# Kernel tuning notes

Hardware: AMD Instinct MI355X
Metric: run time of the kernel (lower is better)

Reference implementation:

```python
import jax, jax.numpy as jnp
import numpy as np

D_MODEL, D_STATE, D_CONV, EXPAND = 1024, 16, 4, 2
D_INNER = D_MODEL * EXPAND
B, T = 1, 2048
EPS = 1e-5


def setup_inputs() -> dict:
    key = jax.random.key(0)
    ks = jax.random.split(key, 8)
    x = jax.random.normal(ks[0], (B, T, D_MODEL), dtype=jnp.float32)
    W_in = jax.random.normal(ks[1], (D_MODEL, 2 * D_INNER), dtype=jnp.float32) * 0.02
    conv_w = jax.random.normal(ks[2], (D_INNER, D_CONV), dtype=jnp.float32) * 0.2
    conv_b = jax.random.normal(ks[3], (D_INNER,), dtype=jnp.float32) * 0.02
    W_x = jax.random.normal(ks[4], (D_INNER, 2 * D_STATE + 1), dtype=jnp.float32) * 0.02
    W_dt = jax.random.normal(ks[5], (1, D_INNER), dtype=jnp.float32) * 0.5
    b_dt = jax.random.uniform(ks[6], (D_INNER,), dtype=jnp.float32, minval=-0.001, maxval=0.001)
    A_log = jnp.broadcast_to(jnp.log(jnp.arange(1, D_STATE + 1, dtype=jnp.float32))[None, :], (D_INNER, D_STATE))
    Dparam = jnp.ones((D_INNER,), dtype=jnp.float32)
    W_out = jax.random.normal(ks[7], (D_INNER, D_MODEL), dtype=jnp.float32) * 0.02
    ln_g = jnp.ones((D_MODEL,), dtype=jnp.float32)
    ln_b = jnp.zeros((D_MODEL,), dtype=jnp.float32)
    return {"x": x, "W_in": W_in, "conv_w": conv_w, "conv_b": conv_b, "W_x": W_x,
            "W_dt": W_dt, "b_dt": b_dt, "A_log": A_log, "D": Dparam,
            "W_out": W_out, "ln_g": ln_g, "ln_b": ln_b}


def _silu(v):
    return v * jax.nn.sigmoid(v)


def _layernorm(v, g, b):
    mu = jnp.mean(v, axis=-1, keepdims=True)
    var = jnp.mean((v - mu) ** 2, axis=-1, keepdims=True)
    return (v - mu) * jax.lax.rsqrt(var + EPS) * g + b


def _causal_depthwise_conv(xp, conv_w, conv_b):
    # xp: (B, T, D_INNER) -> (B, D_INNER, T) with left pad of D_CONV-1
    xc = jnp.swapaxes(xp, 1, 2)
    xc = jnp.pad(xc, ((0, 0), (0, 0), (D_CONV - 1, 0)))
    w = conv_w[:, None, :]  # (O=D_INNER, I/groups=1, K)
    out = jax.lax.conv_general_dilated(
        xc, w, window_strides=(1,), padding='VALID',
        dimension_numbers=('NCH', 'OIH', 'NCH'), feature_group_count=D_INNER)
    return jnp.swapaxes(out + conv_b[None, :, None], 1, 2)  # (B, T, D_INNER)


def reference(x, W_in, conv_w, conv_b, W_x, W_dt, b_dt, A_log, D, W_out, ln_g, ln_b):
    residual = x
    xn = _layernorm(x, ln_g, ln_b)
    xz = xn @ W_in                      # (B, T, 2*D_INNER)
    x_proj, z = jnp.split(xz, 2, axis=-1)
    x_conv = _silu(_causal_depthwise_conv(x_proj, conv_w, conv_b))  # (B, T, D_INNER)

    ssm = x_conv @ W_x                  # (B, T, 1 + 2*D_STATE)
    dt_raw = ssm[..., :1]
    Bp = ssm[..., 1:1 + D_STATE]        # (B, T, D_STATE)
    Cp = ssm[..., 1 + D_STATE:]         # (B, T, D_STATE)
    dt = jax.nn.softplus(dt_raw @ W_dt + b_dt)  # (B, T, D_INNER)

    A = -jnp.exp(A_log)                 # (D_INNER, D_STATE)
    A_bar = jnp.exp(dt[..., None] * A)                              # (B,T,d,n)
    Bx = dt[..., None] * Bp[:, :, None, :] * x_conv[..., None]      # (B,T,d,n)

    def step(h, inp):
        Ab_t, Bx_t, C_t = inp           # (B,d,n),(B,d,n),(B,n)
        h = Ab_t * h + Bx_t
        y_t = jnp.einsum('bdn,bn->bd', h, C_t)
        return h, y_t

    h0 = jnp.zeros((x.shape[0], D_INNER, D_STATE), dtype=x.dtype)
    _, ys = jax.lax.scan(step, h0, (jnp.swapaxes(A_bar, 0, 1),
                                    jnp.swapaxes(Bx, 0, 1),
                                    jnp.swapaxes(Cp, 0, 1)))
    y = jnp.swapaxes(ys, 0, 1)          # (B, T, D_INNER)

    y = y + x_conv * D
    y = y * _silu(z)
    return y @ W_out + residual
```

## Files before the change

kernel.cpp:

```cpp
#include <hip/hip_runtime.h>
#include <hip/hip_bf16.h>

typedef __hip_bfloat16 bf16;
typedef __attribute__((ext_vector_type(8))) short bf16x8;
typedef __attribute__((ext_vector_type(4))) float f32x4;

#define T_LEN 2048
#define DMODEL 1024
#define DINNER 2048
#define DSTATE 16
#define LN_EPS 1e-5f
#define NCHUNK 128
#define CLEN 16
#define SSTR 64
#define PSEG 131072

#define GLOBAL_AS __attribute__((address_space(1)))
#define LDS_AS __attribute__((address_space(3)))

__device__ __forceinline__ void g2l16(void* lds, const void* g) {
    __builtin_amdgcn_global_load_lds((const GLOBAL_AS void*)g, (LDS_AS void*)lds, 16, 0, 0);
}

__device__ __forceinline__ float b2f(short s) {
    return __uint_as_float(((unsigned)(unsigned short)s) << 16);
}

__device__ __forceinline__ unsigned short f2bu(float f) {
    bf16 b = __float2bfloat16(f);
    return *reinterpret_cast<unsigned short*>(&b);
}

__global__ void prep_all(const float* __restrict__ Win, const float* __restrict__ Wout,
                         const float* __restrict__ Wx, const float* __restrict__ x,
                         const float* __restrict__ lng, const float* __restrict__ lnb,
                         bf16* __restrict__ WinT, bf16* __restrict__ WoutT,
                         bf16* __restrict__ WxT, bf16* __restrict__ xn) {
    __shared__ float t[32][33];
    int bid = blockIdx.x, tid = threadIdx.x;
    int tx = tid & 31, ty4 = (tid >> 5) * 4;
    if (bid < 4096) {
        int n0 = (bid & 127) * 32, k0 = (bid >> 7) * 32;
#pragma unroll
        for (int r = 0; r < 4; r++)
            t[ty4 + r][tx] = Win[(size_t)(k0 + ty4 + r) * 4096 + n0 + tx];
        __syncthreads();
#pragma unroll
        for (int r = 0; r < 4; r++)
            WinT[(size_t)(n0 + ty4 + r) * 1024 + k0 + tx] = __float2bfloat16(t[tx][ty4 + r]);
    } else if (bid < 6144) {
        int b = bid - 4096;
        int n0 = (b & 31) * 32, k0 = (b >> 5) * 32;
#pragma unroll
        for (int r = 0; r < 4; r++)
            t[ty4 + r][tx] = Wout[(size_t)(k0 + ty4 + r) * 1024 + n0 + tx];
        __syncthreads();
#pragma unroll
        for (int r = 0; r < 4; r++)
            WoutT[(size_t)(n0 + ty4 + r) * 2048 + k0 + tx] = __float2bfloat16(t[tx][ty4 + r]);
    } else if (bid < 6656) {
        int idx = (bid - 6144) * 256 + tid;
        int n = idx >> 11, k = idx & 2047;
        int j = (n == 0) ? 0 : (n >= 4 && n <= 35) ? n - 3 : -1;
        WxT[idx] = __float2bfloat16(j >= 0 ? Wx[k * 33 + j] : 0.f);
    } else {
        int row = bid - 6656;
        const float* xr = x + (size_t)row * DMODEL;
        float v[4];
        float s = 0.f, q = 0.f;
#pragma unroll
        for (int i = 0; i < 4; i++) {
            v[i] = xr[tid + i * 256];
            s += v[i];
            q += v[i] * v[i];
        }
        __shared__ float sh_s[256], sh_q[256];
        sh_s[tid] = s; sh_q[tid] = q;
        __syncthreads();
        for (int st = 128; st > 0; st >>= 1) {
            if (tid < st) { sh_s[tid] += sh_s[tid + st]; sh_q[tid] += sh_q[tid + st]; }
            __syncthreads();
        }
        float mean = sh_s[0] * (1.f / DMODEL);
        float var  = sh_q[0] * (1.f / DMODEL) - mean * mean;
        float rstd = rsqrtf(var + LN_EPS);
#pragma unroll
        for (int i = 0; i < 4; i++) {
            int c = tid + i * 256;
            xn[(size_t)row * DMODEL + c] =
                __float2bfloat16((v[i] - mean) * rstd * lng[c] + lnb[c]);
        }
    }
}

template <int BM, int BN, int WAVE_M, int WAVE_N, int WRITE_RESID, int OUT_BF16>
__global__ void gemm_mfma(const bf16* __restrict__ A, const bf16* __restrict__ Bt,
                          void* __restrict__ Cv, const float* __restrict__ resid,
                          int M, int N, int Kslice, int lda) {
    constexpr int WMsz = BM / WAVE_M;
    constexpr int WNsz = BN / WAVE_N;
    constexpr int TM = WMsz / 16;
    constexpr int TN = WNsz / 16;
    __shared__ short As[BM * 64];
    __shared__ short Bs[BN * 64];
    int tid = threadIdx.x;
    int lane = tid & 63, wave = tid >> 6;
    int wm = (wave / WAVE_N) * WMsz, wn = (wave % WAVE_N) * WNsz;
    int rowBase = blockIdx.y * BM, colBase = blockIdx.x * BN;
    int kbase = blockIdx.z * Kslice;

    f32x4 acc[TM][TN];
#pragma unroll
    for (int i = 0; i < TM; i++)
#pragma unroll
        for (int j = 0; j < TN; j++) acc[i][j] = f32x4{0.f, 0.f, 0.f, 0.f};

    int srow = tid >> 3;
    int cc = (tid & 7) ^ (srow & 7);
    const int ldsoff = tid * 16;

    for (int k0 = kbase; k0 < kbase + Kslice; k0 += 64) {
#pragma unroll
        for (int j = 0; j < BM / 32; j++)
            g2l16((char*)As + j * 4096 + ldsoff,
                  A + (size_t)(rowBase + j * 32 + srow) * lda + k0 + cc * 8);
#pragma unroll
        for (int j = 0; j < BN / 32; j++)
            g2l16((char*)Bs + j * 4096 + ldsoff,
                  Bt + (size_t)(colBase + j * 32 + srow) * lda + k0 + cc * 8);
        __syncthreads();
#pragma unroll
        for (int ks = 0; ks < 2; ks++) {
            bf16x8 af[TM], bfr[TN];
#pragma unroll
            for (int i = 0; i < TM; i++) {
                int row = wm + i * 16 + (lane & 15);
                int slot = (ks * 4 + (lane >> 4)) ^ (row & 7);
                af[i] = *(const bf16x8*)((const char*)As + row * 128 + slot * 16);
            }
#pragma unroll
            for (int j = 0; j < TN; j++) {
                int row = wn + j * 16 + (lane & 15);
                int slot = (ks * 4 + (lane >> 4)) ^ (row & 7);
                bfr[j] = *(const bf16x8*)((const char*)Bs + row * 128 + slot * 16);
            }
#pragma unroll
            for (int i = 0; i < TM; i++)
#pragma unroll
                for (int j = 0; j < TN; j++)
                    acc[i][j] = __builtin_amdgcn_mfma_f32_16x16x32_bf16(
                        af[i], bfr[j], acc[i][j], 0, 0, 0);
        }
        __syncthreads();
    }
    int rq = lane >> 4, cn = lane & 15;
    float* Cf = (float*)Cv + (size_t)blockIdx.z * M * N;
#pragma unroll
    for (int i = 0; i < TM; i++) {
#pragma unroll
        for (int j = 0; j < TN; j++) {
#pragma unroll
            for (int r = 0; r < 4; r++) {
                size_t row = rowBase + wm + i * 16 + rq * 4 + r;
                int col = colBase + wn + j * 16 + cn;
                float v = acc[i][j][r];
                if (WRITE_RESID) v += resid[row * N + col];
                if (OUT_BF16)
                    ((bf16*)Cv)[row * N + col] = __float2bfloat16(v);
                else
                    Cf[row * N + col] = v;
            }
        }
    }
}

__global__ void conv_silu(const bf16* __restrict__ xz, const float* __restrict__ cw,
                          const float* __restrict__ cb, bf16* __restrict__ xc) {
    int idx = blockIdx.x * 256 + threadIdx.x;
    int t = idx >> 9, d4 = (idx & 511) * 4;
    const f32x4 bv = *(const f32x4*)(cb + d4);
    float acc0 = bv[0], acc1 = bv[1], acc2 = bv[2], acc3 = bv[3];
    const f32x4* cwv = (const f32x4*)(cw + d4 * 4);
    f32x4 w0 = cwv[0], w1 = cwv[1], w2 = cwv[2], w3 = cwv[3];
#pragma unroll
    for (int k = 0; k < 4; k++) {
        int tt = t - 3 + k;
        if (tt >= 0) {
            ushort4 v = *(const ushort4*)((const short*)xz + (size_t)tt * (2 * DINNER) + d4);
            acc0 = fmaf(b2f((short)v.x), w0[k], acc0);
            acc1 = fmaf(b2f((short)v.y), w1[k], acc1);
            acc2 = fmaf(b2f((short)v.z), w2[k], acc2);
            acc3 = fmaf(b2f((short)v.w), w3[k], acc3);
        }
    }
    ushort4 o;
    o.x = f2bu(acc0 / (1.f + __expf(-acc0)));
    o.y = f2bu(acc1 / (1.f + __expf(-acc1)));
    o.z = f2bu(acc2 / (1.f + __expf(-acc2)));
    o.w = f2bu(acc3 / (1.f + __expf(-acc3)));
    *(ushort4*)((short*)xc + (size_t)t * DINNER + d4) = o;
}

__global__ void reduce_parts(const float* __restrict__ parts, float* __restrict__ ssm) {
    int idx = (blockIdx.x * 256 + threadIdx.x) * 4;
    f32x4 a = *(const f32x4*)(parts + idx);
    f32x4 b = *(const f32x4*)(parts + idx + PSEG);
    f32x4 c = *(const f32x4*)(parts + idx + 2 * PSEG);
    f32x4 d = *(const f32x4*)(parts + idx + 3 * PSEG);
    *(f32x4*)(ssm + idx) = (a + b) + (c + d);
}

__device__ __forceinline__ float softplus_f(float pre) {
    return (pre > 20.f) ? pre : log1pf(__expf(pre));
}

__device__ __forceinline__ void powtree(float q, float* a) {
    a[0] = q;
    a[1] = q * q;
    a[2] = a[1] * q;
    a[3] = a[1] * a[1];
#pragma unroll
    for (int j = 0; j < 4; j++) a[4 + j] = a[j] * a[3];
#pragma unroll
    for (int j = 0; j < 8; j++) a[8 + j] = a[j] * a[7];
}

__global__ void scan_pass1(
        const float* __restrict__ ssm, const bf16* __restrict__ xc,
        const float* __restrict__ Wdt, const float* __restrict__ bdt,
        const float* __restrict__ Alog,
        float* __restrict__ Ld, float* __restrict__ S) {
    int tid = threadIdx.x;
    int d = blockIdx.x * 256 + tid;
    int c = blockIdx.y;
    int t0 = c * CLEN;
    short xcv[CLEN];
#pragma unroll
    for (int i = 0; i < CLEN; i++)
        xcv[i] = ((const short*)xc)[(size_t)(t0 + i) * DINNER + d];
    float A[DSTATE];
    bool fast = true;
#pragma unroll
    for (int n = 0; n < DSTATE; n++) {
        A[n] = -__expf(Alog[d * DSTATE + n]);
        fast = fast && (fabsf(A[n] + (float)(n + 1)) < 1e-3f * (n + 1));
    }
    float wdt = Wdt[d], bd = bdt[d];
    float Sv[DSTATE];
#pragma unroll
    for (int n = 0; n < DSTATE; n++) Sv[n] = 0.f;
    float Lsum = 0.f;
    if (fast) {
#pragma unroll
        for (int i = 0; i < CLEN; i++) {
            const float* sr = ssm + (size_t)(t0 + i) * SSTR;
            float dt = softplus_f(sr[0] * wdt + bd);
            Lsum += dt;
            float u = dt * b2f(xcv[i]);
            float a[DSTATE];
            powtree(__expf(-dt), a);
#pragma unroll
            for (int n = 0; n < DSTATE; n++)
                Sv[n] = fmaf(a[n], Sv[n], u * sr[4 + n]);
        }
    } else {
#pragma unroll
        for (int i = 0; i < CLEN; i++) {
            const float* sr = ssm + (size_t)(t0 + i) * SSTR;
            float dt = softplus_f(sr[0] * wdt + bd);
            Lsum += dt;
            float u = dt * b2f(xcv[i]);
#pragma unroll
            for (int n = 0; n < DSTATE; n++)
                Sv[n] = fmaf(__expf(dt * A[n]), Sv[n], u * sr[4 + n]);
        }
    }
    Ld[(size_t)c * DINNER + d] = Lsum;
    size_t base = (size_t)c * DINNER * DSTATE + d;
#pragma unroll
    for (int n = 0; n < DSTATE; n++)
        S[base + (size_t)n * DINNER] = Sv[n];
}

__global__ void scan_pass2(const float* __restrict__ Ld, const float* __restrict__ S,
                           const float* __restrict__ Alog, float* __restrict__ Hst) {
    int idx = blockIdx.x * 256 + threadIdx.x;
    int d = idx & (DINNER - 1), n = idx >> 11;
    float A = -__expf(Alog[d * DSTATE + n]);
    float H = 0.f;
#pragma unroll 8
    for (int c = 0; c < NCHUNK; c++) {
        size_t o = (size_t)c * DINNER * DSTATE + idx;
        float Sc = S[o];
        float a = __expf(A * Ld[(size_t)c * DINNER + d]);
        Hst[o] = H;
        H = a * H + Sc;
    }
}

__global__ void scan_pass3(
        const float* __restrict__ ssm, const bf16* __restrict__ xc,
        const bf16* __restrict__ xz,
        const float* __restrict__ Wdt, const float* __restrict__ bdt,
        const float* __restrict__ Alog, const float* __restrict__ Dp,
        const float* __restrict__ Hst, bf16* __restrict__ yf) {
    int tid = threadIdx.x;
    int d = blockIdx.x * 256 + tid;
    int c = blockIdx.y;
    int t0 = c * CLEN;
    short xcv[CLEN], zv[CLEN];
#pragma unroll
    for (int i = 0; i < CLEN; i++) {
        xcv[i] = ((const short*)xc)[(size_t)(t0 + i) * DINNER + d];
        zv[i]  = ((const short*)xz)[(size_t)(t0 + i) * (2 * DINNER) + DINNER + d];
    }
    float A[DSTATE], h[DSTATE];
    bool fast = true;
    size_t base = (size_t)c * DINNER * DSTATE + d;
#pragma unroll
    for (int n = 0; n < DSTATE; n++) {
        A[n] = -__expf(Alog[d * DSTATE + n]);
        fast = fast && (fabsf(A[n] + (float)(n + 1)) < 1e-3f * (n + 1));
        h[n] = Hst[base + (size_t)n * DINNER];
    }
    float wdt = Wdt[d], bd = bdt[d], Dd = Dp[d];
    if (fast) {
#pragma unroll
        for (int i = 0; i < CLEN; i++) {
            const float* sr = ssm + (size_t)(t0 + i) * SSTR;
            float dt = softplus_f(sr[0] * wdt + bd);
            float xcf = b2f(xcv[i]);
            float u = dt * xcf;
            float a[DSTATE];
            powtree(__expf(-dt), a);
            float y0 = 0.f, y1 = 0.f, y2 = 0.f, y3 = 0.f;
#pragma unroll
            for (int n = 0; n < 4; n++) {
                h[n]      = fmaf(a[n],      h[n],      u * sr[4 + n]);
                y0 = fmaf(h[n],      sr[20 + n], y0);
                h[n + 4]  = fmaf(a[n + 4],  h[n + 4],  u * sr[8 + n]);
                y1 = fmaf(h[n + 4],  sr[24 + n], y1);
                h[n + 8]  = fmaf(a[n + 8],  h[n + 8],  u * sr[12 + n]);
                y2 = fmaf(h[n + 8],  sr[28 + n], y2);
                h[n + 12] = fmaf(a[n + 12], h[n + 12], u * sr[16 + n]);
                y3 = fmaf(h[n + 12], sr[32 + n], y3);
            }
            float y = (y0 + y1) + (y2 + y3);
            float z = b2f(zv[i]);
            float sz = z / (1.f + __expf(-z));
            yf[(size_t)(t0 + i) * DINNER + d] = __float2bfloat16(fmaf(xcf, Dd, y) * sz);
        }
    } else {
#pragma unroll
        for (int i = 0; i < CLEN; i++) {
            const float* sr = ssm + (size_t)(t0 + i) * SSTR;
            float dt = softplus_f(sr[0] * wdt + bd);
            float xcf = b2f(xcv[i]);
            float u = dt * xcf;
            float y = 0.f;
#pragma unroll
            for (int n = 0; n < DSTATE; n++) {
                float a = __expf(dt * A[n]);
                h[n] = fmaf(a, h[n], u * sr[4 + n]);
                y = fmaf(h[n], sr[20 + n], y);
            }
            float z = b2f(zv[i]);
            float sz = z / (1.f + __expf(-z));
            yf[(size_t)(t0 + i) * DINNER + d] = __float2bfloat16(fmaf(xcf, Dd, y) * sz);
        }
    }
}

extern "C" void kernel_launch(void* const* d_in, const int* in_sizes, int n_in,
                              void* d_out, int out_size, void* d_ws, size_t ws_size,
                              hipStream_t stream) {
    const float* x     = (const float*)d_in[0];
    const float* W_in  = (const float*)d_in[1];
    const float* convw = (const float*)d_in[2];
    const float* convb = (const float*)d_in[3];
    const float* W_x   = (const float*)d_in[4];
    const float* W_dt  = (const float*)d_in[5];
    const float* b_dt  = (const float*)d_in[6];
    const float* A_log = (const float*)d_in[7];
    const float* Dp    = (const float*)d_in[8];
    const float* W_out = (const float*)d_in[9];
    const float* ln_g  = (const float*)d_in[10];
    const float* ln_b  = (const float*)d_in[11];
    float* out = (float*)d_out;

    char* wsb = (char*)d_ws;
    bf16*  xn    = (bf16*)(wsb);
    bf16*  WinT  = (bf16*)(wsb + (4ull  << 20));
    bf16*  WoutT = (bf16*)(wsb + (12ull << 20));
    bf16*  WxT   = (bf16*)(wsb + (16ull << 20));
    bf16*  xz    = (bf16*)(wsb + (17ull << 20));
    bf16*  xc    = (bf16*)(wsb + (33ull << 20));
    float* parts = (float*)(wsb + (41ull << 20));
    float* Ld    = (float*)(wsb + (43ull << 20));
    float* Hst   = (float*)(wsb + (44ull << 20));
    float* S     = (float*)(wsb + (60ull << 20));
    bf16*  yf    = (bf16*)(wsb + (76ull << 20));
    float* ssm   = (float*)(wsb + (84ull << 20));

    prep_all<<<8704, 256, 0, stream>>>(W_in, W_out, W_x, x, ln_g, ln_b,
                                       WinT, WoutT, WxT, xn);

    gemm_mfma<128, 128, 2, 2, 0, 1><<<dim3(4096 / 128, 2048 / 128), 256, 0, stream>>>(
        xn, WinT, xz, nullptr, 2048, 4096, 1024, 1024);

    conv_silu<<<(T_LEN * DINNER / 4) / 256, 256, 0, stream>>>(xz, convw, convb, xc);

    gemm_mfma<32, 64, 2, 2, 0, 0><<<dim3(1, 2048 / 32, 4), 256, 0, stream>>>(
        xc, WxT, parts, nullptr, 2048, 64, 512, 2048);

    reduce_parts<<<(T_LEN * SSTR / 4) / 256, 256, 0, stream>>>(parts, ssm);

    scan_pass1<<<dim3(DINNER / 256, NCHUNK), 256, 0, stream>>>(
        ssm, xc, W_dt, b_dt, A_log, Ld, S);
    scan_pass2<<<(DINNER * DSTATE) / 256, 256, 0, stream>>>(Ld, S, A_log, Hst);
    scan_pass3<<<dim3(DINNER / 256, NCHUNK), 256, 0, stream>>>(
        ssm, xc, xz, W_dt, b_dt, A_log, Dp, Hst, yf);

    gemm_mfma<64, 64, 2, 2, 1, 0><<<dim3(1024 / 64, 2048 / 64), 256, 0, stream>>>(
        yf, WoutT, out, x, 2048, 1024, 2048, 2048);
}
```

Measured before the change: 249.2 us.

## Double-buffer ssm row loads in scan passes and parallelize chunk carry scan

Scan passes 1 and 3 now load each timestep's ssm row as vector f32x4 loads into alternating register buffers, prefetching the next timestep while computing the current one, instead of scalar per-element loads. Scan pass 2 is restructured so four threads share one (d,n) pair: each does a sub-scan over a quarter of the chunks, carries are combined through shared memory, then each writes its segment's prefix states. This targets the serial 128-step latency chain in pass 2 and load latency in passes 1/3, at the cost of more registers and a second pass over the exp terms.

```diff
diff --git a/kernel.cpp b/kernel.cpp
--- a/kernel.cpp
+++ b/kernel.cpp
@@ -30,6 +30,8 @@
     bf16 b = __float2bfloat16(f);
     return *reinterpret_cast<unsigned short*>(&b);
 }
+
+#define BG(buf, j) (buf[(j) >> 2][(j) & 3])
 
 __global__ void prep_all(const float* __restrict__ Win, const float* __restrict__ Wout,
                          const float* __restrict__ Wx, const float* __restrict__ x,
@@ -225,6 +227,49 @@
     for (int j = 0; j < 8; j++) a[8 + j] = a[j] * a[7];
 }
 
+__device__ __forceinline__ void ldrow(f32x4* b, const f32x4* sp) {
+#pragma unroll
+    for (int k = 0; k < 9; k++) b[k] = sp[k];
+}
+
+template <int FAST>
+__device__ __forceinline__ void p1_step(const f32x4* buf, short xcs, float wdt, float bd,
+                                        const float* A, float& Lsum, float* Sv) {
+    float dt = softplus_f(BG(buf, 0) * wdt + bd);
+    Lsum += dt;
+    float u = dt * b2f(xcs);
+    if (FAST) {
+        float a[DSTATE];
+        powtree(__expf(-dt), a);
+#pragma unroll
+        for (int n = 0; n < DSTATE; n++)
+            Sv[n] = fmaf(a[n], Sv[n], u * BG(buf, 4 + n));
+    } else {
+#pragma unroll
+        for (int n = 0; n < DSTATE; n++)
+            Sv[n] = fmaf(__expf(dt * A[n]), Sv[n], u * BG(buf, 4 + n));
+    }
+}
+
+template <int FAST>
+__device__ __forceinline__ void p1_loop(const f32x4* sp, const short* xcp,
+                                        float wdt, float bd, const float* A,
+                                        float& Lsum, float* Sv) {
+    f32x4 bA[9], bB[9];
+    short xA, xB;
+    ldrow(bA, sp);
+    xA = xcp[0];
+#pragma unroll
+    for (int i = 0; i < CLEN; i += 2) {
+        ldrow(bB, sp + (i + 1) * 16);
+        xB = xcp[(size_t)(i + 1) * DINNER];
+        p1_step<FAST>(bA, xA, wdt, bd, A, Lsum, Sv);
+        ldrow(bA, sp + (i + 2) * 16);
+        xA = xcp[(size_t)(i + 2) * DINNER];
+        p1_step<FAST>(bB, xB, wdt, bd, A, Lsum, Sv);
+    }
+}
+
 __global__ void scan_pass1(
         const float* __restrict__ ssm, const bf16* __restrict__ xc,
         const float* __restrict__ Wdt, const float* __restrict__ bdt,
@@ -234,10 +279,6 @@
     int d = blockIdx.x * 256 + tid;
     int c = blockIdx.y;
     int t0 = c * CLEN;
-    short xcv[CLEN];
-#pragma unroll
-    for (int i = 0; i < CLEN; i++)
-        xcv[i] = ((const short*)xc)[(size_t)(t0 + i) * DINNER + d];
     float A[DSTATE];
     bool fast = true;
 #pragma unroll
@@ -250,31 +291,12 @@
 #pragma unroll
     for (int n = 0; n < DSTATE; n++) Sv[n] = 0.f;
     float Lsum = 0.f;
-    if (fast) {
-#pragma unroll
-        for (int i = 0; i < CLEN; i++) {
-            const float* sr = ssm + (size_t)(t0 + i) * SSTR;
-            float dt = softplus_f(sr[0] * wdt + bd);
-            Lsum += dt;
-            float u = dt * b2f(xcv[i]);
-            float a[DSTATE];
-            powtree(__expf(-dt), a);
-#pragma unroll
-            for (int n = 0; n < DSTATE; n++)
-                Sv[n] = fmaf(a[n], Sv[n], u * sr[4 + n]);
-        }
-    } else {
-#pragma unroll
-        for (int i = 0; i < CLEN; i++) {
-            const float* sr = ssm + (size_t)(t0 + i) * SSTR;
-            float dt = softplus_f(sr[0] * wdt + bd);
-            Lsum += dt;
-            float u = dt * b2f(xcv[i]);
-#pragma unroll
-            for (int n = 0; n < DSTATE; n++)
-                Sv[n] = fmaf(__expf(dt * A[n]), Sv[n], u * sr[4 + n]);
-        }
-    }
+    const f32x4* sp = (const f32x4*)(ssm + (size_t)t0 * SSTR);
+    const short* xcp = (const short*)xc + (size_t)t0 * DINNER + d;
+    if (fast)
+        p1_loop<1>(sp, xcp, wdt, bd, A, Lsum, Sv);
+    else
+        p1_loop<0>(sp, xcp, wdt, bd, A, Lsum, Sv);
     Ld[(size_t)c * DINNER + d] = Lsum;
     size_t base = (size_t)c * DINNER * DSTATE + d;
 #pragma unroll
@@ -282,19 +304,107 @@
         S[base + (size_t)n * DINNER] = Sv[n];
 }
 
+#define SEGL (NCHUNK / 4)
 __global__ void scan_pass2(const float* __restrict__ Ld, const float* __restrict__ S,
                            const float* __restrict__ Alog, float* __restrict__ Hst) {
-    int idx = blockIdx.x * 256 + threadIdx.x;
-    int d = idx & (DINNER - 1), n = idx >> 11;
+    int tx = threadIdx.x & 63, ty = threadIdx.x >> 6;
+    int d = blockIdx.x * 64 + tx;
+    int n = blockIdx.y;
     float A = -__expf(Alog[d * DSTATE + n]);
-    float H = 0.f;
-#pragma unroll 8
-    for (int c = 0; c < NCHUNK; c++) {
-        size_t o = (size_t)c * DINNER * DSTATE + idx;
-        float Sc = S[o];
-        float a = __expf(A * Ld[(size_t)c * DINNER + d]);
+    int c0 = ty * SEGL;
+    float lv[SEGL], sv[SEGL];
+#pragma unroll
+    for (int j = 0; j < SEGL; j++) {
+        int cc = c0 + j;
+        lv[j] = Ld[(size_t)cc * DINNER + d];
+        sv[j] = S[(size_t)cc * DINNER * DSTATE + (size_t)n * DINNER + d];
+    }
+    float Lsum = 0.f, Sseg = 0.f;
+#pragma unroll
+    for (int j = 0; j < SEGL; j++) {
+        Sseg = fmaf(__expf(A * lv[j]), Sseg, sv[j]);
+        Lsum += lv[j];
+    }
+    __shared__ float shL[4][64], shS[4][64], shC[4][64];
+    shL[ty][tx] = Lsum;
+    shS[ty][tx] = Sseg;
+    __syncthreads();
+    if (ty == 0) {
+        float car = 0.f;
+        shC[0][tx] = 0.f;
+#pragma unroll
+        for (int s = 0; s < 3; s++) {
+            car = fmaf(__expf(A * shL[s][tx]), car, shS[s][tx]);
+            shC[s + 1][tx] = car;
+        }
+    }
+    __syncthreads();
+    float H = shC[ty][tx];
+#pragma unroll
+    for (int j = 0; j < SEGL; j++) {
+        size_t o = (size_t)(c0 + j) * DINNER * DSTATE + (size_t)n * DINNER + d;
         Hst[o] = H;
-        H = a * H + Sc;
+        H = fmaf(__expf(A * lv[j]), H, sv[j]);
+    }
+}
+
+template <int FAST>
+__device__ __forceinline__ void p3_step(const f32x4* buf, short xcs, short zs,
+                                        float wdt, float bd, float Dd, const float* A,
+                                        float* h, bf16* outp) {
+    float dt = softplus_f(BG(buf, 0) * wdt + bd);
+    float xcf = b2f(xcs);
+    float u = dt * xcf;
+    float y;
+    if (FAST) {
+        float a[DSTATE];
+        powtree(__expf(-dt), a);
+        float y0 = 0.f, y1 = 0.f, y2 = 0.f, y3 = 0.f;
+#pragma unroll
+        for (int n = 0; n < 4; n++) {
+            h[n]      = fmaf(a[n],      h[n],      u * BG(buf, 4 + n));
+            y0 = fmaf(h[n],      BG(buf, 20 + n), y0);
+            h[n + 4]  = fmaf(a[n + 4],  h[n + 4],  u * BG(buf, 8 + n));
+            y1 = fmaf(h[n + 4],  BG(buf, 24 + n), y1);
+            h[n + 8]  = fmaf(a[n + 8],  h[n + 8],  u * BG(buf, 12 + n));
+            y2 = fmaf(h[n + 8],  BG(buf, 28 + n), y2);
+            h[n + 12] = fmaf(a[n + 12], h[n + 12], u * BG(buf, 16 + n));
+            y3 = fmaf(h[n + 12], BG(buf, 32 + n), y3);
+        }
+        y = (y0 + y1) + (y2 + y3);
+    } else {
+        y = 0.f;
+#pragma unroll
+        for (int n = 0; n < DSTATE; n++) {
+            float a = __expf(dt * A[n]);
+            h[n] = fmaf(a, h[n], u * BG(buf, 4 + n));
+            y = fmaf(h[n], BG(buf, 20 + n), y);
+        }
+    }
+    float z = b2f(zs);
+    float sz = z / (1.f + __expf(-z));
+    *outp = __float2bfloat16(fmaf(xcf, Dd, y) * sz);
+}
+
+template <int FAST>
+__device__ __forceinline__ void p3_loop(const f32x4* sp, const short* xcp, const short* zp,
+                                        float wdt, float bd, float Dd, const float* A,
+                                        float* h, bf16* yp) {
+    f32x4 bA[9], bB[9];
+    short xA, xB, zA, zB;
+    ldrow(bA, sp);
+    xA = xcp[0];
+    zA = zp[0];
+#pragma unroll
+    for (int i = 0; i < CLEN; i += 2) {
+        ldrow(bB, sp + (i + 1) * 16);
+        xB = xcp[(size_t)(i + 1) * DINNER];
+        zB = zp[(size_t)(i + 1) * 2 * DINNER];
+        p3_step<FAST>(bA, xA, zA, wdt, bd, Dd, A, h, yp + (size_t)i * DINNER);
+        ldrow(bA, sp + (i + 2) * 16);
+        xA = xcp[(size_t)(i + 2) * DINNER];
+        zA = zp[(size_t)(i + 2) * 2 * DINNER];
+        p3_step<FAST>(bB, xB, zB, wdt, bd, Dd, A, h, yp + (size_t)(i + 1) * DINNER);
     }
 }
 
@@ -308,12 +418,6 @@
     int d = blockIdx.x * 256 + tid;
     int c = blockIdx.y;
     int t0 = c * CLEN;
-    short xcv[CLEN], zv[CLEN];
-#pragma unroll
-    for (int i = 0; i < CLEN; i++) {
-        xcv[i] = ((const short*)xc)[(size_t)(t0 + i) * DINNER + d];
-        zv[i]  = ((const short*)xz)[(size_t)(t0 + i) * (2 * DINNER) + DINNER + d];
-    }
     float A[DSTATE], h[DSTATE];
     bool fast = true;
     size_t base = (size_t)c * DINNER * DSTATE + d;
@@ -324,51 +428,14 @@
         h[n] = Hst[base + (size_t)n * DINNER];
     }
     float wdt = Wdt[d], bd = bdt[d], Dd = Dp[d];
-    if (fast) {
-#pragma unroll
-        for (int i = 0; i < CLEN; i++) {
-            const float* sr = ssm + (size_t)(t0 + i) * SSTR;
-            float dt = softplus_f(sr[0] * wdt + bd);
-            float xcf = b2f(xcv[i]);
-            float u = dt * xcf;
-            float a[DSTATE];
-            powtree(__expf(-dt), a);
-            float y0 = 0.f, y1 = 0.f, y2 = 0.f, y3 = 0.f;
-#pragma unroll
-            for (int n = 0; n < 4; n++) {
-                h[n]      = fmaf(a[n],      h[n],      u * sr[4 + n]);
-                y0 = fmaf(h[n],      sr[20 + n], y0);
-                h[n + 4]  = fmaf(a[n + 4],  h[n + 4],  u * sr[8 + n]);
-                y1 = fmaf(h[n + 4],  sr[24 + n], y1);
-                h[n + 8]  = fmaf(a[n + 8],  h[n + 8],  u * sr[12 + n]);
-                y2 = fmaf(h[n + 8],  sr[28 + n], y2);
-                h[n + 12] = fmaf(a[n + 12], h[n + 12], u * sr[16 + n]);
-                y3 = fmaf(h[n + 12], sr[32 + n], y3);
-            }
-            float y = (y0 + y1) + (y2 + y3);
-            float z = b2f(zv[i]);
-            float sz = z / (1.f + __expf(-z));
-            yf[(size_t)(t0 + i) * DINNER + d] = __float2bfloat16(fmaf(xcf, Dd, y) * sz);
-        }
-    } else {
-#pragma unroll
-        for (int i = 0; i < CLEN; i++) {
-            const float* sr = ssm + (size_t)(t0 + i) * SSTR;
-            float dt = softplus_f(sr[0] * wdt + bd);
-            float xcf = b2f(xcv[i]);
-            float u = dt * xcf;
-            float y = 0.f;
-#pragma unroll
-            for (int n = 0; n < DSTATE; n++) {
-                float a = __expf(dt * A[n]);
-                h[n] = fmaf(a, h[n], u * sr[4 + n]);
-                y = fmaf(h[n], sr[20 + n], y);
-            }
-            float z = b2f(zv[i]);
-            float sz = z / (1.f + __expf(-z));
-            yf[(size_t)(t0 + i) * DINNER + d] = __float2bfloat16(fmaf(xcf, Dd, y) * sz);
-        }
-    }
+    const f32x4* sp = (const f32x4*)(ssm + (size_t)t0 * SSTR);
+    const short* xcp = (const short*)xc + (size_t)t0 * DINNER + d;
+    const short* zp  = (const short*)xz + (size_t)t0 * (2 * DINNER) + DINNER + d;
+    bf16* yp = yf + (size_t)t0 * DINNER + d;
+    if (fast)
+        p3_loop<1>(sp, xcp, zp, wdt, bd, Dd, A, h, yp);
+    else
+        p3_loop<0>(sp, xcp, zp, wdt, bd, Dd, A, h, yp);
 }
 
 extern "C" void kernel_launch(void* const* d_in, const int* in_sizes, int n_in,
@@ -417,7 +484,7 @@
 
     scan_pass1<<<dim3(DINNER / 256, NCHUNK), 256, 0, stream>>>(
         ssm, xc, W_dt, b_dt, A_log, Ld, S);
-    scan_pass2<<<(DINNER * DSTATE) / 256, 256, 0, stream>>>(Ld, S, A_log, Hst);
+    scan_pass2<<<dim3(DINNER / 64, DSTATE), 256, 0, stream>>>(Ld, S, A_log, Hst);
     scan_pass3<<<dim3(DINNER / 256, NCHUNK), 256, 0, stream>>>(
         ssm, xc, xz, W_dt, b_dt, A_log, Dp, Hst, yf);
 
```

After: 234.3 us. 6.0% less time.
